# Performance work log

Measured on AMD Instinct MI355X. Metric: run time of the kernel, lower is better.

Reference implementation:

```python
import jax, jax.numpy as jnp
import numpy as np

D_MODEL = 768
D_STATE = 16
D_CONV = 4
EXPAND = 2
INNER = EXPAND * D_MODEL  # 1536
BATCH = 2
SEQLEN = 2048


def setup_inputs() -> dict:
    key = jax.random.key(0)
    ks = jax.random.split(key, 8)
    s = 0.02
    return {
        "hidden_states": jax.random.normal(ks[0], (BATCH, SEQLEN, D_MODEL), jnp.float32),
        "in_proj_w": jax.random.normal(ks[1], (2 * INNER, D_MODEL), jnp.float32) * (D_MODEL ** -0.5),
        "out_proj_w": jax.random.normal(ks[2], (D_MODEL, INNER), jnp.float32) * (INNER ** -0.5),
        "dt_proj_w": jax.random.normal(ks[3], (INNER, INNER), jnp.float32) * (INNER ** -0.5),
        "dt_proj_b": jnp.zeros((INNER,), jnp.float32),
        "conv_w": jax.random.normal(ks[4], (INNER, D_CONV), jnp.float32) * s,
        "conv_b": jnp.zeros((INNER,), jnp.float32),
        "A_log": jnp.zeros((INNER, D_STATE), jnp.float32),
        "B_param": jax.random.normal(ks[5], (INNER, D_STATE), jnp.float32) * s,
        "C_param": jax.random.normal(ks[6], (INNER, D_STATE), jnp.float32) * s,
        "D_param": jnp.ones((INNER,), jnp.float32),
        "dt_bias": jnp.zeros((INNER,), jnp.float32),
    }


def reference(hidden_states, in_proj_w, out_proj_w, dt_proj_w, dt_proj_b,
              conv_w, conv_b, A_log, B_param, C_param, D_param, dt_bias):
    # in_proj: (B, L, d_model) -> (B, L, 2*inner); split into projected / gate
    xz = jnp.einsum('bld,od->blo', hidden_states, in_proj_w)
    proj, gate = jnp.split(xz, 2, axis=-1)
    x = jnp.transpose(proj, (0, 2, 1))  # (B, inner, L) channel-first

    # depthwise causal conv (left-pad d_conv-1) + bias + SiLU
    conv = jax.lax.conv_general_dilated(
        x, conv_w[:, None, :], window_strides=(1,),
        padding=[(D_CONV - 1, 0)], feature_group_count=INNER,
        dimension_numbers=('NCH', 'OIH', 'NCH'))
    u = jax.nn.silu(conv + conv_b[None, :, None])  # (B, inner, L)

    # dt projection (1x1 linear on channel-first) + softplus(dt + dt_bias)
    delta = jnp.einsum('oc,bcl->bol', dt_proj_w, u) + dt_proj_b[None, :, None]
    dt = jax.nn.softplus(delta + dt_bias[None, :, None])  # (B, inner, L)

    A = -jnp.exp(A_log)  # (inner, d_state)
    # discretize: dA = exp(dt * A), dBu = dt * u * B   -> (B, inner, L, N)
    dA = jnp.exp(dt[..., None] * A[None, :, None, :])
    dBu = (dt * u)[..., None] * B_param[None, :, None, :]

    dA_t = jnp.moveaxis(dA, 2, 0)    # (L, B, inner, N)
    dBu_t = jnp.moveaxis(dBu, 2, 0)  # (L, B, inner, N)

    def step(h, inp):
        a_t, b_t = inp
        h = a_t * h + b_t                      # (B, inner, N)
        y = jnp.einsum('bdn,dn->bd', h, C_param)
        return h, y

    h0 = jnp.zeros(dA_t.shape[1:], dA.dtype)
    _, ys = jax.lax.scan(step, h0, (dA_t, dBu_t))  # ys: (L, B, inner)
    y = jnp.transpose(ys, (1, 2, 0))               # (B, inner, L)

    z = jnp.transpose(gate, (0, 2, 1))             # (B, inner, L)
    y = (y + D_param[None, :, None] * u) * jax.nn.silu(z)

    # out_proj: (B, inner, L) -> (B, L, d_model)
    return jnp.einsum('bdl,od->blo', y, out_proj_w)
```

## Files before the change

kernel.cpp:

```cpp
#include <hip/hip_runtime.h>
#include <cstdint>
#include <cstddef>

#define D_MODEL 768
#define D_STATE 16
#define D_CONV  4
#define INNER   1536
#define BATCH   2
#define SEQLEN  2048
#define M_TOK   (BATCH * SEQLEN)
#define NCH     (BATCH * INNER)
#define NCHUNK  128
#define CL      (SEQLEN / NCHUNK)

typedef unsigned short u16;
typedef __attribute__((ext_vector_type(4))) unsigned short us4;
typedef __attribute__((ext_vector_type(8))) short bf8;
typedef __attribute__((ext_vector_type(4))) float f32x4;
typedef __attribute__((ext_vector_type(4))) int i32x4;

#define INV254 (1.f / 254.f)

__device__ __forceinline__ u16 f2bf(float f) {
    uint32_t x = __float_as_uint(f);
    return (u16)((x + 0x7fffu + ((x >> 16) & 1u)) >> 16);
}
__device__ __forceinline__ float bf2f(u16 h) {
    return __uint_as_float(((uint32_t)h) << 16);
}
__device__ __forceinline__ int pk8(float a, float b, float c, float d) {
    return ((int)a & 0xff) | (((int)b & 0xff) << 8) |
           (((int)c & 0xff) << 16) | (((int)d & 0xff) << 24);
}

__global__ __launch_bounds__(256) void prep_all(
    const float* __restrict__ hs, int8_t* __restrict__ hs1, int8_t* __restrict__ hs0, float* __restrict__ sc_hs,
    const float* __restrict__ iw, int8_t* __restrict__ iw1, int8_t* __restrict__ iw0, float* __restrict__ sc_iw,
    const float* __restrict__ dw, int8_t* __restrict__ dw1, int8_t* __restrict__ dw0, float* __restrict__ sc_dw,
    const float* __restrict__ ow, u16* __restrict__ owh, u16* __restrict__ owl)
{
    const int blk = blockIdx.x;
    const int tid = threadIdx.x;

    if (blk >= M_TOK + 2 * INNER + INNER) {
        const int j = (blk - (M_TOK + 3 * INNER)) * 256 + tid;
        const int n4 = D_MODEL * INNER / 4;
        if (j >= n4) return;
        const float4 v = ((const float4*)ow)[j];
        us4 h, l;
        h.x = f2bf(v.x); l.x = f2bf(v.x - bf2f(h.x));
        h.y = f2bf(v.y); l.y = f2bf(v.y - bf2f(h.y));
        h.z = f2bf(v.z); l.z = f2bf(v.z - bf2f(h.z));
        h.w = f2bf(v.w); l.w = f2bf(v.w - bf2f(h.w));
        ((us4*)owh)[j] = h;
        ((us4*)owl)[j] = l;
        return;
    }

    const float* src; int8_t* q1; int8_t* q0; float* sc; int K; int row;
    if (blk < M_TOK) {
        src = hs; q1 = hs1; q0 = hs0; sc = sc_hs; K = D_MODEL; row = blk;
    } else if (blk < M_TOK + 2 * INNER) {
        src = iw; q1 = iw1; q0 = iw0; sc = sc_iw; K = D_MODEL; row = blk - M_TOK;
    } else {
        src = dw; q1 = dw1; q0 = dw0; sc = sc_dw; K = INNER; row = blk - M_TOK - 2 * INNER;
    }

    const float* r = src + (size_t)row * K;
    float mx = 0.f;
    for (int i = tid * 4; i < K; i += 1024) {
        const float4 v = *(const float4*)(r + i);
        mx = fmaxf(mx, fmaxf(fmaxf(fabsf(v.x), fabsf(v.y)),
                             fmaxf(fabsf(v.z), fabsf(v.w))));
    }
#pragma unroll
    for (int off = 1; off < 64; off <<= 1)
        mx = fmaxf(mx, __shfl_xor(mx, off, 64));
    __shared__ float red[4];
    if ((tid & 63) == 0) red[tid >> 6] = mx;
    __syncthreads();
    const float rm = fmaxf(fmaxf(red[0], red[1]), fmaxf(red[2], red[3]));
    const float q = rm > 0.f ? 127.f / rm : 0.f;

    for (int i = tid * 4; i < K; i += 1024) {
        const float4 v = *(const float4*)(r + i);
        float s1[4], s0[4];
        const float xv[4] = {v.x, v.y, v.z, v.w};
#pragma unroll
        for (int e = 0; e < 4; ++e) {
            const float t = xv[e] * q;
            s1[e] = rintf(t);
            s0[e] = rintf((t - s1[e]) * 254.f);
        }
        const size_t o = ((size_t)row * K + i) >> 2;
        ((int*)q1)[o] = pk8(s1[0], s1[1], s1[2], s1[3]);
        ((int*)q0)[o] = pk8(s0[0], s0[1], s0[2], s0[3]);
    }
    if (tid == 0) sc[row] = rm * (1.f / 127.f);
}

template <int MODE, int FRM, int FRN>
__global__ __launch_bounds__(256) void gemm_i8(
    const int8_t* __restrict__ A1g, const int8_t* __restrict__ A0g,
    const int8_t* __restrict__ B1g, const int8_t* __restrict__ B0g,
    const float* __restrict__ scA, const float* __restrict__ scB,
    void* __restrict__ Cv, const float* __restrict__ bias1,
    const float* __restrict__ bias2, int M, int N, int K)
{
    constexpr int BM = FRM * 32;
    constexpr int BN = FRN * 32;
    constexpr int SBUF = (BM + BN) * 128;
    __shared__ __align__(16) char smem[2 * SBUF];

    const int tid = threadIdx.x;
    const int w = tid >> 6;
    const int lane = tid & 63;

    const int gx = gridDim.x;
    const int nwg = gx * gridDim.y;
    int f = blockIdx.y * gx + blockIdx.x;
    f = (f & 7) * (nwg >> 3) + (f >> 3);
    const int bm = (f / gx) * BM;
    const int bn = (f % gx) * BN;

    const int wm = (w >> 1) * (FRM * 16);
    const int wn = (w & 1) * (FRN * 16);

    const int g8 = lane & 7;
    const int r8 = lane >> 3;
    const int srcg = g8 ^ r8;
    const int sbyte = (srcg & 3) * 16;
    const bool use_lo = (srcg & 4) != 0;

    const int8_t* pA[FRM];
    const int8_t* pB[FRN];
#pragma unroll
    for (int c = 0; c < FRM; ++c) {
        const int row = w * (FRM * 8) + c * 8 + r8;
        pA[c] = (use_lo ? A0g : A1g) + (size_t)(bm + row) * K + sbyte;
    }
#pragma unroll
    for (int c = 0; c < FRN; ++c) {
        const int row = w * (FRN * 8) + c * 8 + r8;
        pB[c] = (use_lo ? B0g : B1g) + (size_t)(bn + row) * K + sbyte;
    }

    i32x4 acc1[FRM][FRN] = {};
    i32x4 acc2[FRM][FRN] = {};
    const int fr = lane & 15;
    const int gk = lane >> 4;
    const int ghi = gk ^ (fr & 7);

    const int aoff1 = (wm + fr) * 128 + ghi * 16;
    const int aoff0 = (wm + fr) * 128 + (ghi ^ 4) * 16;
    const int boff1 = BM * 128 + (wn + fr) * 128 + ghi * 16;
    const int boff0 = BM * 128 + (wn + fr) * 128 + (ghi ^ 4) * 16;
    const char* const S0 = smem;
    const char* const S1 = smem + SBUF;

    const int nt = K >> 6;

#define STAGE_ALL(sb, kt)                                                           \
    {                                                                               \
        _Pragma("unroll")                                                           \
        for (int c = 0; c < FRM; ++c)                                               \
            __builtin_amdgcn_global_load_lds(                                       \
                (const __attribute__((address_space(1))) void*)(pA[c] + (kt)),      \
                (__attribute__((address_space(3))) void*)((char*)(sb) + (w * FRM + c) * 1024), \
                16, 0, 0);                                                          \
        _Pragma("unroll")                                                           \
        for (int c = 0; c < FRN; ++c)                                               \
            __builtin_amdgcn_global_load_lds(                                       \
                (const __attribute__((address_space(1))) void*)(pB[c] + (kt)),      \
                (__attribute__((address_space(3))) void*)((char*)(sb) + BM * 128 + (w * FRN + c) * 1024), \
                16, 0, 0);                                                          \
    }

#define WAIT_COUNTED()                                                              \
    if constexpr (FRM + FRN == 8) { asm volatile("s_waitcnt vmcnt(8)" ::: "memory"); } \
    else if constexpr (FRM + FRN == 6) { asm volatile("s_waitcnt vmcnt(6)" ::: "memory"); } \
    else { asm volatile("s_waitcnt vmcnt(4)" ::: "memory"); }

#define COMPUTE(S)                                                                  \
    {                                                                               \
        i32x4 a1[FRM], a0[FRM], b1[FRN], b0[FRN];                                   \
        _Pragma("unroll")                                                           \
        for (int i = 0; i < FRM; ++i) {                                             \
            a1[i] = *(const i32x4*)((S) + aoff1 + i * 2048);                        \
            a0[i] = *(const i32x4*)((S) + aoff0 + i * 2048);                        \
        }                                                                           \
        _Pragma("unroll")                                                           \
        for (int j = 0; j < FRN; ++j) {                                             \
            b1[j] = *(const i32x4*)((S) + boff1 + j * 2048);                        \
            b0[j] = *(const i32x4*)((S) + boff0 + j * 2048);                        \
        }                                                                           \
        _Pragma("unroll")                                                           \
        for (int i = 0; i < FRM; ++i)                                               \
            _Pragma("unroll")                                                       \
            for (int j = 0; j < FRN; ++j) {                                         \
                acc1[i][j] = __builtin_amdgcn_mfma_i32_16x16x64_i8(a1[i], b1[j], acc1[i][j], 0, 0, 0); \
                acc2[i][j] = __builtin_amdgcn_mfma_i32_16x16x64_i8(a1[i], b0[j], acc2[i][j], 0, 0, 0); \
                acc2[i][j] = __builtin_amdgcn_mfma_i32_16x16x64_i8(a0[i], b1[j], acc2[i][j], 0, 0, 0); \
            }                                                                       \
    }

    STAGE_ALL(S0, 0)

    for (int t = 0; t < nt; t += 2) {
        STAGE_ALL(S1, (t + 1) * 64)
        WAIT_COUNTED()
        __builtin_amdgcn_s_barrier();
        __builtin_amdgcn_sched_barrier(0);
        __builtin_amdgcn_s_setprio(1);
        COMPUTE(S0)
        __builtin_amdgcn_s_setprio(0);
        __builtin_amdgcn_sched_barrier(0);
        __builtin_amdgcn_s_barrier();

        const int k2 = (t + 2 < nt) ? (t + 2) * 64 : (nt - 1) * 64;
        STAGE_ALL(S0, k2)
        WAIT_COUNTED()
        __builtin_amdgcn_s_barrier();
        __builtin_amdgcn_sched_barrier(0);
        __builtin_amdgcn_s_setprio(1);
        COMPUTE(S1)
        __builtin_amdgcn_s_setprio(0);
        __builtin_amdgcn_sched_barrier(0);
        __builtin_amdgcn_s_barrier();
    }
#undef STAGE_ALL
#undef WAIT_COUNTED
#undef COMPUTE

    const int r0 = (lane >> 4) * 4;
#pragma unroll
    for (int i = 0; i < FRM; ++i) {
        const int row0 = bm + wm + i * 16 + r0;
        float sA[4];
#pragma unroll
        for (int r = 0; r < 4; ++r) sA[r] = scA[row0 + r];
#pragma unroll
        for (int j = 0; j < FRN; ++j) {
            const int col = bn + wn + j * 16 + fr;
            const float sB = scB[col];
            float add = 0.f;
            if constexpr (MODE == 1) add = bias1[col] + bias2[col];
#pragma unroll
            for (int r = 0; r < 4; ++r) {
                float v = ((float)acc1[i][j][r] +
                           (float)acc2[i][j][r] * INV254) * (sA[r] * sB);
                if constexpr (MODE == 1) {
                    const float xx = v + add;
                    v = (xx > 20.f) ? xx : log1pf(expf(xx));
                    ((u16*)Cv)[(size_t)(row0 + r) * N + col] = f2bf(v);
                } else {
                    ((float*)Cv)[(size_t)(row0 + r) * N + col] = v;
                }
            }
        }
    }
}

template <int MODE, int FRM, int FRN>
__global__ __launch_bounds__(256) void gemm_mfma(
    const u16* __restrict__ Ah_g, const u16* __restrict__ Al_g,
    const u16* __restrict__ Bh_g, const u16* __restrict__ Bl_g,
    float* __restrict__ C, const float* __restrict__ bias1,
    const float* __restrict__ bias2, int M, int N, int K)
{
    constexpr int BM = FRM * 32;
    constexpr int BN = FRN * 32;
    constexpr int SBUF = (BM + BN) * 128;
    __shared__ __align__(16) char smem[2 * SBUF];

    const int tid = threadIdx.x;
    const int w = tid >> 6;
    const int lane = tid & 63;

    const int gx = gridDim.x;
    const int nwg = gx * gridDim.y;
    int f = blockIdx.y * gx + blockIdx.x;
    f = (f & 7) * (nwg >> 3) + (f >> 3);
    const int bm = (f / gx) * BM;
    const int bn = (f % gx) * BN;

    const int wm = (w >> 1) * (FRM * 16);
    const int wn = (w & 1) * (FRN * 16);

    const int g8 = lane & 7;
    const int r8 = lane >> 3;
    const int srcg = g8 ^ r8;
    const int scol = (srcg & 3) * 8;
    const bool use_lo = (srcg & 4) != 0;

    const u16* pA[FRM];
    const u16* pB[FRN];
#pragma unroll
    for (int c = 0; c < FRM; ++c) {
        const int row = w * (FRM * 8) + c * 8 + r8;
        pA[c] = (use_lo ? Al_g : Ah_g) + (size_t)(bm + row) * K + scol;
    }
#pragma unroll
    for (int c = 0; c < FRN; ++c) {
        const int row = w * (FRN * 8) + c * 8 + r8;
        pB[c] = (use_lo ? Bl_g : Bh_g) + (size_t)(bn + row) * K + scol;
    }

    f32x4 acc[FRM][FRN] = {};
    const int fr = lane & 15;
    const int gk = lane >> 4;
    const int ghi = gk ^ (fr & 7);

    const int aoff_h = (wm + fr) * 128 + ghi * 16;
    const int aoff_l = (wm + fr) * 128 + (ghi ^ 4) * 16;
    const int boff_h = BM * 128 + (wn + fr) * 128 + ghi * 16;
    const int boff_l = BM * 128 + (wn + fr) * 128 + (ghi ^ 4) * 16;
    const char* const S0 = smem;
    const char* const S1 = smem + SBUF;

    const int nt = K >> 5;

#define STAGE_ALL(sb, kt)                                                           \
    {                                                                               \
        _Pragma("unroll")                                                           \
        for (int c = 0; c < FRM; ++c)                                               \
            __builtin_amdgcn_global_load_lds(                                       \
                (const __attribute__((address_space(1))) void*)(pA[c] + (kt)),      \
                (__attribute__((address_space(3))) void*)((char*)(sb) + (w * FRM + c) * 1024), \
                16, 0, 0);                                                          \
        _Pragma("unroll")                                                           \
        for (int c = 0; c < FRN; ++c)                                               \
            __builtin_amdgcn_global_load_lds(                                       \
                (const __attribute__((address_space(1))) void*)(pB[c] + (kt)),      \
                (__attribute__((address_space(3))) void*)((char*)(sb) + BM * 128 + (w * FRN + c) * 1024), \
                16, 0, 0);                                                          \
    }

#define WAIT_COUNTED()                                                              \
    if constexpr (FRM + FRN == 8) { asm volatile("s_waitcnt vmcnt(8)" ::: "memory"); } \
    else if constexpr (FRM + FRN == 6) { asm volatile("s_waitcnt vmcnt(6)" ::: "memory"); } \
    else { asm volatile("s_waitcnt vmcnt(4)" ::: "memory"); }

#define COMPUTE(S)                                                                  \
    {                                                                               \
        bf8 ah[FRM], al[FRM], bh[FRN], bl[FRN];                                     \
        _Pragma("unroll")                                                           \
        for (int i = 0; i < FRM; ++i) {                                             \
            ah[i] = *(const bf8*)((S) + aoff_h + i * 2048);                         \
            al[i] = *(const bf8*)((S) + aoff_l + i * 2048);                         \
        }                                                                           \
        _Pragma("unroll")                                                           \
        for (int j = 0; j < FRN; ++j) {                                             \
            bh[j] = *(const bf8*)((S) + boff_h + j * 2048);                         \
            bl[j] = *(const bf8*)((S) + boff_l + j * 2048);                         \
        }                                                                           \
        _Pragma("unroll")                                                           \
        for (int i = 0; i < FRM; ++i)                                               \
            _Pragma("unroll")                                                       \
            for (int j = 0; j < FRN; ++j) {                                         \
                acc[i][j] = __builtin_amdgcn_mfma_f32_16x16x32_bf16(ah[i], bh[j], acc[i][j], 0, 0, 0); \
                acc[i][j] = __builtin_amdgcn_mfma_f32_16x16x32_bf16(ah[i], bl[j], acc[i][j], 0, 0, 0); \
                acc[i][j] = __builtin_amdgcn_mfma_f32_16x16x32_bf16(al[i], bh[j], acc[i][j], 0, 0, 0); \
            }                                                                       \
    }

    STAGE_ALL(S0, 0)

    for (int t = 0; t < nt; t += 2) {
        STAGE_ALL(S1, (t + 1) * 32)
        WAIT_COUNTED()
        __builtin_amdgcn_s_barrier();
        __builtin_amdgcn_sched_barrier(0);
        __builtin_amdgcn_s_setprio(1);
        COMPUTE(S0)
        __builtin_amdgcn_s_setprio(0);
        __builtin_amdgcn_sched_barrier(0);
        __builtin_amdgcn_s_barrier();

        const int k2 = (t + 2 < nt) ? (t + 2) * 32 : (nt - 1) * 32;
        STAGE_ALL(S0, k2)
        WAIT_COUNTED()
        __builtin_amdgcn_s_barrier();
        __builtin_amdgcn_sched_barrier(0);
        __builtin_amdgcn_s_setprio(1);
        COMPUTE(S1)
        __builtin_amdgcn_s_setprio(0);
        __builtin_amdgcn_sched_barrier(0);
        __builtin_amdgcn_s_barrier();
    }
#undef STAGE_ALL
#undef WAIT_COUNTED
#undef COMPUTE

    const int r0 = (lane >> 4) * 4;
#pragma unroll
    for (int i = 0; i < FRM; ++i) {
        const int row0 = bm + wm + i * 16 + r0;
#pragma unroll
        for (int j = 0; j < FRN; ++j) {
            const int col = bn + wn + j * 16 + fr;
            float add = 0.f;
            if constexpr (MODE == 1) add = bias1[col] + bias2[col];
#pragma unroll
            for (int r = 0; r < 4; ++r) {
                float v = acc[i][j][r];
                if constexpr (MODE == 1) {
                    const float xx = v + add;
                    v = (xx > 20.f) ? xx : log1pf(expf(xx));
                }
                C[(size_t)(row0 + r) * N + col] = v;
            }
        }
    }
}

__global__ __launch_bounds__(384) void conv_silu_quant(
    const float* __restrict__ xz, const float* __restrict__ cw,
    const float* __restrict__ cb, int8_t* __restrict__ u1,
    int8_t* __restrict__ u0, float* __restrict__ su)
{
    const int m = blockIdx.x;
    const int tid = threadIdx.x;
    const int c4 = tid * 4;
    const int b = m >> 11;
    const int l = m & (SEQLEN - 1);

    float wt[4][4];
#pragma unroll
    for (int i = 0; i < 4; ++i) {
        const float4 wv = *(const float4*)&cw[(c4 + i) * 4];
        wt[i][0] = wv.x; wt[i][1] = wv.y; wt[i][2] = wv.z; wt[i][3] = wv.w;
    }
    const float4 bias = *(const float4*)&cb[c4];
    float a[4] = {bias.x, bias.y, bias.z, bias.w};

#pragma unroll
    for (int j = 0; j < 4; ++j) {
        const int ll = l - 3 + j;
        if (ll >= 0) {
            const float4 x = *(const float4*)&xz[(size_t)(b * SEQLEN + ll) * (2 * INNER) + c4];
            a[0] = fmaf(x.x, wt[0][j], a[0]);
            a[1] = fmaf(x.y, wt[1][j], a[1]);
            a[2] = fmaf(x.z, wt[2][j], a[2]);
            a[3] = fmaf(x.w, wt[3][j], a[3]);
        }
    }
    float o[4];
#pragma unroll
    for (int i = 0; i < 4; ++i) o[i] = a[i] / (1.f + __expf(-a[i]));

    float mx = fmaxf(fmaxf(fabsf(o[0]), fabsf(o[1])),
                     fmaxf(fabsf(o[2]), fabsf(o[3])));
#pragma unroll
    for (int off = 1; off < 64; off <<= 1)
        mx = fmaxf(mx, __shfl_xor(mx, off, 64));
    __shared__ float red[6];
    if ((tid & 63) == 0) red[tid >> 6] = mx;
    __syncthreads();
    float rm = red[0];
#pragma unroll
    for (int i = 1; i < 6; ++i) rm = fmaxf(rm, red[i]);
    const float q = rm > 0.f ? 127.f / rm : 0.f;

    float s1[4], s0[4];
#pragma unroll
    for (int e = 0; e < 4; ++e) {
        const float t = o[e] * q;
        s1[e] = rintf(t);
        s0[e] = rintf((t - s1[e]) * 254.f);
    }
    const size_t vi = ((size_t)m * INNER + c4) >> 2;
    ((int*)u1)[vi] = pk8(s1[0], s1[1], s1[2], s1[3]);
    ((int*)u0)[vi] = pk8(s0[0], s0[1], s0[2], s0[3]);
    if (tid == 0) su[m] = rm * (1.f / 127.f);
}

__global__ __launch_bounds__(256) void scan_pass1(
    const u16* __restrict__ dtb, const int8_t* __restrict__ u1,
    const int8_t* __restrict__ u0, const float* __restrict__ su,
    const float* __restrict__ A_log, const float* __restrict__ Bp,
    float* __restrict__ hend, float* __restrict__ Sdt)
{
    const int ch = blockIdx.x * 256 + threadIdx.x;
    const int c = blockIdx.y;
    const int b = (ch >= INNER) ? 1 : 0;
    const int d = ch - b * INNER;

    float A2[D_STATE], Bn[D_STATE];
#pragma unroll
    for (int n = 0; n < D_STATE; n += 4) {
        const float4 av = *(const float4*)&A_log[d * D_STATE + n];
        const float4 bv = *(const float4*)&Bp[d * D_STATE + n];
        A2[n+0] = -expf(av.x) * 1.44269504f; Bn[n+0] = bv.x;
        A2[n+1] = -expf(av.y) * 1.44269504f; Bn[n+1] = bv.y;
        A2[n+2] = -expf(av.z) * 1.44269504f; Bn[n+2] = bv.z;
        A2[n+3] = -expf(av.w) * 1.44269504f; Bn[n+3] = bv.w;
    }

    const size_t base = (size_t)(b * SEQLEN + c * CL) * INNER + d;
    const u16* dtp = dtb + base;
    const int8_t* u1p = u1 + base;
    const int8_t* u0p = u0 + base;
    const float* sup = su + (b * SEQLEN + c * CL);

    float h[D_STATE] = {};
    float S = 0.f;

    float dtv = bf2f(dtp[0]);
    float uv = fmaf((float)u0p[0], INV254, (float)u1p[0]) * sup[0];

    for (int l = 0; l < CL; ++l) {
        float dtn = 0.f, un = 0.f;
        if (l + 1 < CL) {
            dtn = bf2f(dtp[(size_t)(l + 1) * INNER]);
            un = fmaf((float)u0p[(size_t)(l + 1) * INNER], INV254,
                      (float)u1p[(size_t)(l + 1) * INNER]) * sup[l + 1];
        }
        const float dtu = dtv * uv;
        S += dtv;
#pragma unroll
        for (int n = 0; n < D_STATE; ++n) {
            const float dA = exp2f(dtv * A2[n]);
            h[n] = fmaf(dA, h[n], dtu * Bn[n]);
        }
        dtv = dtn; uv = un;
    }

#pragma unroll
    for (int n = 0; n < D_STATE; ++n)
        hend[((size_t)c * D_STATE + n) * NCH + ch] = h[n];
    Sdt[(size_t)c * NCH + ch] = S;
}

__global__ __launch_bounds__(256) void scan_combine(
    const float* __restrict__ hend, const float* __restrict__ Sdt,
    const float* __restrict__ A_log, float* __restrict__ h0all)
{
    const int idx = blockIdx.x * 256 + threadIdx.x;
    const int n = idx / NCH;
    const int ch = idx - n * NCH;
    const int b = (ch >= INNER) ? 1 : 0;
    const int d = ch - b * INNER;
    const float A2 = -expf(A_log[d * D_STATE + n]) * 1.44269504f;

    float h0 = 0.f;
    for (int c = 0; c < NCHUNK; ++c) {
        const size_t o = ((size_t)c * D_STATE + n) * NCH + ch;
        h0all[o] = h0;
        const float P = exp2f(A2 * Sdt[(size_t)c * NCH + ch]);
        h0 = fmaf(P, h0, hend[o]);
    }
}

__global__ __launch_bounds__(256) void scan_pass2(
    const u16* __restrict__ dtb, const int8_t* __restrict__ u1,
    const int8_t* __restrict__ u0, const float* __restrict__ su,
    const float* __restrict__ xz, const float* __restrict__ A_log,
    const float* __restrict__ Bp, const float* __restrict__ Cp,
    const float* __restrict__ Dp, const float* __restrict__ h0all,
    u16* __restrict__ ygh, u16* __restrict__ ygl)
{
    const int ch = blockIdx.x * 256 + threadIdx.x;
    const int c = blockIdx.y;
    const int b = (ch >= INNER) ? 1 : 0;
    const int d = ch - b * INNER;

    float A2[D_STATE], Bn[D_STATE], Cn[D_STATE];
#pragma unroll
    for (int n = 0; n < D_STATE; n += 4) {
        const float4 av = *(const float4*)&A_log[d * D_STATE + n];
        const float4 bv = *(const float4*)&Bp[d * D_STATE + n];
        const float4 cv = *(const float4*)&Cp[d * D_STATE + n];
        A2[n+0] = -expf(av.x) * 1.44269504f; Bn[n+0] = bv.x; Cn[n+0] = cv.x;
        A2[n+1] = -expf(av.y) * 1.44269504f; Bn[n+1] = bv.y; Cn[n+1] = cv.y;
        A2[n+2] = -expf(av.z) * 1.44269504f; Bn[n+2] = bv.z; Cn[n+2] = cv.z;
        A2[n+3] = -expf(av.w) * 1.44269504f; Bn[n+3] = bv.w; Cn[n+3] = cv.w;
    }
    const float Dd = Dp[d];

    float h[D_STATE];
#pragma unroll
    for (int n = 0; n < D_STATE; ++n)
        h[n] = h0all[((size_t)c * D_STATE + n) * NCH + ch];

    const size_t base = (size_t)(b * SEQLEN + c * CL) * INNER + d;
    const u16* dtp = dtb + base;
    const int8_t* u1p = u1 + base;
    const int8_t* u0p = u0 + base;
    const float* sup = su + (b * SEQLEN + c * CL);
    const float* zp = xz + (size_t)(b * SEQLEN + c * CL) * (2 * INNER) + INNER + d;
    u16* yhp = ygh + base;
    u16* ylp = ygl + base;

    float dtv = bf2f(dtp[0]);
    float uv = fmaf((float)u0p[0], INV254, (float)u1p[0]) * sup[0];
    float zv = zp[0];

    for (int l = 0; l < CL; ++l) {
        float dtn = 0.f, un = 0.f, zn = 0.f;
        if (l + 1 < CL) {
            dtn = bf2f(dtp[(size_t)(l + 1) * INNER]);
            un = fmaf((float)u0p[(size_t)(l + 1) * INNER], INV254,
                      (float)u1p[(size_t)(l + 1) * INNER]) * sup[l + 1];
            zn = zp[(size_t)(l + 1) * (2 * INNER)];
        }
        const float dtu = dtv * uv;
        float y = 0.f;
#pragma unroll
        for (int n = 0; n < D_STATE; ++n) {
            const float dA = exp2f(dtv * A2[n]);
            h[n] = fmaf(dA, h[n], dtu * Bn[n]);
            y = fmaf(h[n], Cn[n], y);
        }
        const float sig = 1.f / (1.f + __expf(-zv));
        const float val = (y + Dd * uv) * (zv * sig);
        const u16 hv = f2bf(val);
        yhp[(size_t)l * INNER] = hv;
        ylp[(size_t)l * INNER] = f2bf(val - bf2f(hv));
        dtv = dtn; uv = un; zv = zn;
    }
}

extern "C" void kernel_launch(void* const* d_in, const int* in_sizes, int n_in,
                              void* d_out, int out_size, void* d_ws, size_t ws_size,
                              hipStream_t stream)
{
    const float* hs      = (const float*)d_in[0];
    const float* in_w    = (const float*)d_in[1];
    const float* out_w   = (const float*)d_in[2];
    const float* dt_w    = (const float*)d_in[3];
    const float* dt_b    = (const float*)d_in[4];
    const float* conv_w  = (const float*)d_in[5];
    const float* conv_b  = (const float*)d_in[6];
    const float* A_log   = (const float*)d_in[7];
    const float* Bp      = (const float*)d_in[8];
    const float* Cp      = (const float*)d_in[9];
    const float* Dp      = (const float*)d_in[10];
    const float* dt_bias = (const float*)d_in[11];
    float* out = (float*)d_out;

    float* xz    = (float*)d_ws;
    float* hend  = xz + (size_t)M_TOK * 2 * INNER;
    float* Sdt   = hend + (size_t)NCHUNK * D_STATE * NCH;
    float* h0all = Sdt + (size_t)NCHUNK * NCH;
    float* su_u  = h0all + (size_t)NCHUNK * D_STATE * NCH;
    float* sc_hs = su_u + M_TOK;
    float* sc_iw = sc_hs + M_TOK;
    float* sc_dw = sc_iw + 2 * INNER;
    u16* dtb = (u16*)(sc_dw + INNER);
    u16* ygh = dtb + (size_t)M_TOK * INNER;
    u16* ygl = ygh + (size_t)M_TOK * INNER;
    u16* owh = ygl + (size_t)M_TOK * INNER;
    u16* owl = owh + (size_t)D_MODEL * INNER;
    int8_t* hs1 = (int8_t*)(owl + (size_t)D_MODEL * INNER);
    int8_t* hs0 = hs1 + (size_t)M_TOK * D_MODEL;
    int8_t* iw1 = hs0 + (size_t)M_TOK * D_MODEL;
    int8_t* iw0 = iw1 + (size_t)2 * INNER * D_MODEL;
    int8_t* dw1 = iw0 + (size_t)2 * INNER * D_MODEL;
    int8_t* dw0 = dw1 + (size_t)INNER * INNER;
    int8_t* u1  = dw0 + (size_t)INNER * INNER;
    int8_t* u0  = u1 + (size_t)M_TOK * INNER;

    const dim3 blk(256);

    {
        const int nq = M_TOK + 2 * INNER + INNER;
        const int nc = (D_MODEL * INNER / 4 + 255) / 256;
        prep_all<<<dim3(nq + nc), blk, 0, stream>>>(
            hs, hs1, hs0, sc_hs, in_w, iw1, iw0, sc_iw,
            dt_w, dw1, dw0, sc_dw, out_w, owh, owl);
    }

    gemm_i8<0, 4, 4><<<dim3(2 * INNER / 128, M_TOK / 128), blk, 0, stream>>>(
        hs1, hs0, iw1, iw0, sc_hs, sc_iw, xz, nullptr, nullptr,
        M_TOK, 2 * INNER, D_MODEL);

    conv_silu_quant<<<dim3(M_TOK), dim3(384), 0, stream>>>(
        xz, conv_w, conv_b, u1, u0, su_u);

    gemm_i8<1, 4, 2><<<dim3(INNER / 64, M_TOK / 128), blk, 0, stream>>>(
        u1, u0, dw1, dw0, su_u, sc_dw, dtb, dt_b, dt_bias,
        M_TOK, INNER, INNER);

    scan_pass1<<<dim3(NCH / 256, NCHUNK), blk, 0, stream>>>(
        dtb, u1, u0, su_u, A_log, Bp, hend, Sdt);
    scan_combine<<<dim3((D_STATE * NCH) / 256), blk, 0, stream>>>(
        hend, Sdt, A_log, h0all);
    scan_pass2<<<dim3(NCH / 256, NCHUNK), blk, 0, stream>>>(
        dtb, u1, u0, su_u, xz, A_log, Bp, Cp, Dp, h0all, ygh, ygl);

    gemm_mfma<0, 2, 2><<<dim3(D_MODEL / 64, M_TOK / 64), blk, 0, stream>>>(
        ygh, ygl, owh, owl, out, nullptr, nullptr, M_TOK, D_MODEL, INNER);
}
```

Before: 306.0 us.

## Switch out_proj GEMM from split-bf16 MFMA to two-level int8 GEMM

```diff
diff --git a/kernel.cpp b/kernel.cpp
--- a/kernel.cpp
+++ b/kernel.cpp
@@ -15,7 +15,6 @@
 
 typedef unsigned short u16;
 typedef __attribute__((ext_vector_type(4))) unsigned short us4;
-typedef __attribute__((ext_vector_type(8))) short bf8;
 typedef __attribute__((ext_vector_type(4))) float f32x4;
 typedef __attribute__((ext_vector_type(4))) int i32x4;
 
@@ -33,40 +32,11 @@
            (((int)c & 0xff) << 16) | (((int)d & 0xff) << 24);
 }
 
-__global__ __launch_bounds__(256) void prep_all(
-    const float* __restrict__ hs, int8_t* __restrict__ hs1, int8_t* __restrict__ hs0, float* __restrict__ sc_hs,
-    const float* __restrict__ iw, int8_t* __restrict__ iw1, int8_t* __restrict__ iw0, float* __restrict__ sc_iw,
-    const float* __restrict__ dw, int8_t* __restrict__ dw1, int8_t* __restrict__ dw0, float* __restrict__ sc_dw,
-    const float* __restrict__ ow, u16* __restrict__ owh, u16* __restrict__ owl)
-{
-    const int blk = blockIdx.x;
-    const int tid = threadIdx.x;
-
-    if (blk >= M_TOK + 2 * INNER + INNER) {
-        const int j = (blk - (M_TOK + 3 * INNER)) * 256 + tid;
-        const int n4 = D_MODEL * INNER / 4;
-        if (j >= n4) return;
-        const float4 v = ((const float4*)ow)[j];
-        us4 h, l;
-        h.x = f2bf(v.x); l.x = f2bf(v.x - bf2f(h.x));
-        h.y = f2bf(v.y); l.y = f2bf(v.y - bf2f(h.y));
-        h.z = f2bf(v.z); l.z = f2bf(v.z - bf2f(h.z));
-        h.w = f2bf(v.w); l.w = f2bf(v.w - bf2f(h.w));
-        ((us4*)owh)[j] = h;
-        ((us4*)owl)[j] = l;
-        return;
-    }
-
-    const float* src; int8_t* q1; int8_t* q0; float* sc; int K; int row;
-    if (blk < M_TOK) {
-        src = hs; q1 = hs1; q0 = hs0; sc = sc_hs; K = D_MODEL; row = blk;
-    } else if (blk < M_TOK + 2 * INNER) {
-        src = iw; q1 = iw1; q0 = iw0; sc = sc_iw; K = D_MODEL; row = blk - M_TOK;
-    } else {
-        src = dw; q1 = dw1; q0 = dw0; sc = sc_dw; K = INNER; row = blk - M_TOK - 2 * INNER;
-    }
-
-    const float* r = src + (size_t)row * K;
+__device__ __forceinline__ void rowquant_body(
+    const float* __restrict__ r, int8_t* __restrict__ q1,
+    int8_t* __restrict__ q0, float* __restrict__ sc,
+    int K, size_t rowbase, int tid)
+{
     float mx = 0.f;
     for (int i = tid * 4; i < K; i += 1024) {
         const float4 v = *(const float4*)(r + i);
@@ -92,11 +62,42 @@
             s1[e] = rintf(t);
             s0[e] = rintf((t - s1[e]) * 254.f);
         }
-        const size_t o = ((size_t)row * K + i) >> 2;
+        const size_t o = (rowbase + i) >> 2;
         ((int*)q1)[o] = pk8(s1[0], s1[1], s1[2], s1[3]);
         ((int*)q0)[o] = pk8(s0[0], s0[1], s0[2], s0[3]);
     }
-    if (tid == 0) sc[row] = rm * (1.f / 127.f);
+    if (tid == 0) *sc = rm * (1.f / 127.f);
+}
+
+__global__ __launch_bounds__(256) void prep_all(
+    const float* __restrict__ hs, int8_t* __restrict__ hs1, int8_t* __restrict__ hs0, float* __restrict__ sc_hs,
+    const float* __restrict__ iw, int8_t* __restrict__ iw1, int8_t* __restrict__ iw0, float* __restrict__ sc_iw,
+    const float* __restrict__ dw, int8_t* __restrict__ dw1, int8_t* __restrict__ dw0, float* __restrict__ sc_dw,
+    const float* __restrict__ ow, int8_t* __restrict__ ow1, int8_t* __restrict__ ow0, float* __restrict__ sc_ow)
+{
+    const int blk = blockIdx.x;
+    const int tid = threadIdx.x;
+    const float* src; int8_t* q1; int8_t* q0; float* sc; int K; int row;
+    if (blk < M_TOK) {
+        src = hs; q1 = hs1; q0 = hs0; sc = sc_hs; K = D_MODEL; row = blk;
+    } else if (blk < M_TOK + 2 * INNER) {
+        src = iw; q1 = iw1; q0 = iw0; sc = sc_iw; K = D_MODEL; row = blk - M_TOK;
+    } else if (blk < M_TOK + 3 * INNER) {
+        src = dw; q1 = dw1; q0 = dw0; sc = sc_dw; K = INNER; row = blk - M_TOK - 2 * INNER;
+    } else {
+        src = ow; q1 = ow1; q0 = ow0; sc = sc_ow; K = INNER; row = blk - M_TOK - 3 * INNER;
+    }
+    rowquant_body(src + (size_t)row * K, q1, q0, sc + row, K,
+                  (size_t)row * K, tid);
+}
+
+__global__ __launch_bounds__(256) void rowquant_yg(
+    const float* __restrict__ src, int8_t* __restrict__ q1,
+    int8_t* __restrict__ q0, float* __restrict__ sc)
+{
+    const int row = blockIdx.x;
+    rowquant_body(src + (size_t)row * INNER, q1, q0, sc + row, INNER,
+                  (size_t)row * INNER, threadIdx.x);
 }
 
 template <int MODE, int FRM, int FRN>
@@ -261,159 +262,6 @@
     }
 }
 
-template <int MODE, int FRM, int FRN>
-__global__ __launch_bounds__(256) void gemm_mfma(
-    const u16* __restrict__ Ah_g, const u16* __restrict__ Al_g,
-    const u16* __restrict__ Bh_g, const u16* __restrict__ Bl_g,
-    float* __restrict__ C, const float* __restrict__ bias1,
-    const float* __restrict__ bias2, int M, int N, int K)
-{
-    constexpr int BM = FRM * 32;
-    constexpr int BN = FRN * 32;
-    constexpr int SBUF = (BM + BN) * 128;
-    __shared__ __align__(16) char smem[2 * SBUF];
-
-    const int tid = threadIdx.x;
-    const int w = tid >> 6;
-    const int lane = tid & 63;
-
-    const int gx = gridDim.x;
-    const int nwg = gx * gridDim.y;
-    int f = blockIdx.y * gx + blockIdx.x;
-    f = (f & 7) * (nwg >> 3) + (f >> 3);
-    const int bm = (f / gx) * BM;
-    const int bn = (f % gx) * BN;
-
-    const int wm = (w >> 1) * (FRM * 16);
-    const int wn = (w & 1) * (FRN * 16);
-
-    const int g8 = lane & 7;
-    const int r8 = lane >> 3;
-    const int srcg = g8 ^ r8;
-    const int scol = (srcg & 3) * 8;
-    const bool use_lo = (srcg & 4) != 0;
-
-    const u16* pA[FRM];
-    const u16* pB[FRN];
-#pragma unroll
-    for (int c = 0; c < FRM; ++c) {
-        const int row = w * (FRM * 8) + c * 8 + r8;
-        pA[c] = (use_lo ? Al_g : Ah_g) + (size_t)(bm + row) * K + scol;
-    }
-#pragma unroll
-    for (int c = 0; c < FRN; ++c) {
-        const int row = w * (FRN * 8) + c * 8 + r8;
-        pB[c] = (use_lo ? Bl_g : Bh_g) + (size_t)(bn + row) * K + scol;
-    }
-
-    f32x4 acc[FRM][FRN] = {};
-    const int fr = lane & 15;
-    const int gk = lane >> 4;
-    const int ghi = gk ^ (fr & 7);
-
-    const int aoff_h = (wm + fr) * 128 + ghi * 16;
-    const int aoff_l = (wm + fr) * 128 + (ghi ^ 4) * 16;
-    const int boff_h = BM * 128 + (wn + fr) * 128 + ghi * 16;
-    const int boff_l = BM * 128 + (wn + fr) * 128 + (ghi ^ 4) * 16;
-    const char* const S0 = smem;
-    const char* const S1 = smem + SBUF;
-
-    const int nt = K >> 5;
-
-#define STAGE_ALL(sb, kt)                                                           \
-    {                                                                               \
-        _Pragma("unroll")                                                           \
-        for (int c = 0; c < FRM; ++c)                                               \
-            __builtin_amdgcn_global_load_lds(                                       \
-                (const __attribute__((address_space(1))) void*)(pA[c] + (kt)),      \
-                (__attribute__((address_space(3))) void*)((char*)(sb) + (w * FRM + c) * 1024), \
-                16, 0, 0);                                                          \
-        _Pragma("unroll")                                                           \
-        for (int c = 0; c < FRN; ++c)                                               \
-            __builtin_amdgcn_global_load_lds(                                       \
-                (const __attribute__((address_space(1))) void*)(pB[c] + (kt)),      \
-                (__attribute__((address_space(3))) void*)((char*)(sb) + BM * 128 + (w * FRN + c) * 1024), \
-                16, 0, 0);                                                          \
-    }
-
-#define WAIT_COUNTED()                                                              \
-    if constexpr (FRM + FRN == 8) { asm volatile("s_waitcnt vmcnt(8)" ::: "memory"); } \
-    else if constexpr (FRM + FRN == 6) { asm volatile("s_waitcnt vmcnt(6)" ::: "memory"); } \
-    else { asm volatile("s_waitcnt vmcnt(4)" ::: "memory"); }
-
-#define COMPUTE(S)                                                                  \
-    {                                                                               \
-        bf8 ah[FRM], al[FRM], bh[FRN], bl[FRN];                                     \
-        _Pragma("unroll")                                                           \
-        for (int i = 0; i < FRM; ++i) {                                             \
-            ah[i] = *(const bf8*)((S) + aoff_h + i * 2048);                         \
-            al[i] = *(const bf8*)((S) + aoff_l + i * 2048);                         \
-        }                                                                           \
-        _Pragma("unroll")                                                           \
-        for (int j = 0; j < FRN; ++j) {                                             \
-            bh[j] = *(const bf8*)((S) + boff_h + j * 2048);                         \
-            bl[j] = *(const bf8*)((S) + boff_l + j * 2048);                         \
-        }                                                                           \
-        _Pragma("unroll")                                                           \
-        for (int i = 0; i < FRM; ++i)                                               \
-            _Pragma("unroll")                                                       \
-            for (int j = 0; j < FRN; ++j) {                                         \
-                acc[i][j] = __builtin_amdgcn_mfma_f32_16x16x32_bf16(ah[i], bh[j], acc[i][j], 0, 0, 0); \
-                acc[i][j] = __builtin_amdgcn_mfma_f32_16x16x32_bf16(ah[i], bl[j], acc[i][j], 0, 0, 0); \
-                acc[i][j] = __builtin_amdgcn_mfma_f32_16x16x32_bf16(al[i], bh[j], acc[i][j], 0, 0, 0); \
-            }                                                                       \
-    }
-
-    STAGE_ALL(S0, 0)
-
-    for (int t = 0; t < nt; t += 2) {
-        STAGE_ALL(S1, (t + 1) * 32)
-        WAIT_COUNTED()
-        __builtin_amdgcn_s_barrier();
-        __builtin_amdgcn_sched_barrier(0);
-        __builtin_amdgcn_s_setprio(1);
-        COMPUTE(S0)
-        __builtin_amdgcn_s_setprio(0);
-        __builtin_amdgcn_sched_barrier(0);
-        __builtin_amdgcn_s_barrier();
-
-        const int k2 = (t + 2 < nt) ? (t + 2) * 32 : (nt - 1) * 32;
-        STAGE_ALL(S0, k2)
-        WAIT_COUNTED()
-        __builtin_amdgcn_s_barrier();
-        __builtin_amdgcn_sched_barrier(0);
-        __builtin_amdgcn_s_setprio(1);
-        COMPUTE(S1)
-        __builtin_amdgcn_s_setprio(0);
-        __builtin_amdgcn_sched_barrier(0);
-        __builtin_amdgcn_s_barrier();
-    }
-#undef STAGE_ALL
-#undef WAIT_COUNTED
-#undef COMPUTE
-
-    const int r0 = (lane >> 4) * 4;
-#pragma unroll
-    for (int i = 0; i < FRM; ++i) {
-        const int row0 = bm + wm + i * 16 + r0;
-#pragma unroll
-        for (int j = 0; j < FRN; ++j) {
-            const int col = bn + wn + j * 16 + fr;
-            float add = 0.f;
-            if constexpr (MODE == 1) add = bias1[col] + bias2[col];
-#pragma unroll
-            for (int r = 0; r < 4; ++r) {
-                float v = acc[i][j][r];
-                if constexpr (MODE == 1) {
-                    const float xx = v + add;
-                    v = (xx > 20.f) ? xx : log1pf(expf(xx));
-                }
-                C[(size_t)(row0 + r) * N + col] = v;
-            }
-        }
-    }
-}
-
 __global__ __launch_bounds__(384) void conv_silu_quant(
     const float* __restrict__ xz, const float* __restrict__ cw,
     const float* __restrict__ cb, int8_t* __restrict__ u1,
@@ -558,7 +406,7 @@
     const float* __restrict__ xz, const float* __restrict__ A_log,
     const float* __restrict__ Bp, const float* __restrict__ Cp,
     const float* __restrict__ Dp, const float* __restrict__ h0all,
-    u16* __restrict__ ygh, u16* __restrict__ ygl)
+    float* __restrict__ yg)
 {
     const int ch = blockIdx.x * 256 + threadIdx.x;
     const int c = blockIdx.y;
@@ -589,8 +437,7 @@
     const int8_t* u0p = u0 + base;
     const float* sup = su + (b * SEQLEN + c * CL);
     const float* zp = xz + (size_t)(b * SEQLEN + c * CL) * (2 * INNER) + INNER + d;
-    u16* yhp = ygh + base;
-    u16* ylp = ygl + base;
+    float* ygp = yg + base;
 
     float dtv = bf2f(dtp[0]);
     float uv = fmaf((float)u0p[0], INV254, (float)u1p[0]) * sup[0];
@@ -613,10 +460,7 @@
             y = fmaf(h[n], Cn[n], y);
         }
         const float sig = 1.f / (1.f + __expf(-zv));
-        const float val = (y + Dd * uv) * (zv * sig);
-        const u16 hv = f2bf(val);
-        yhp[(size_t)l * INNER] = hv;
-        ylp[(size_t)l * INNER] = f2bf(val - bf2f(hv));
+        ygp[(size_t)l * INNER] = (y + Dd * uv) * (zv * sig);
         dtv = dtn; uv = un; zv = zn;
     }
 }
@@ -643,35 +487,34 @@
     float* hend  = xz + (size_t)M_TOK * 2 * INNER;
     float* Sdt   = hend + (size_t)NCHUNK * D_STATE * NCH;
     float* h0all = Sdt + (size_t)NCHUNK * NCH;
-    float* su_u  = h0all + (size_t)NCHUNK * D_STATE * NCH;
+    float* yg    = h0all + (size_t)NCHUNK * D_STATE * NCH;
+    float* su_u  = yg + (size_t)M_TOK * INNER;
     float* sc_hs = su_u + M_TOK;
     float* sc_iw = sc_hs + M_TOK;
     float* sc_dw = sc_iw + 2 * INNER;
-    u16* dtb = (u16*)(sc_dw + INNER);
-    u16* ygh = dtb + (size_t)M_TOK * INNER;
-    u16* ygl = ygh + (size_t)M_TOK * INNER;
-    u16* owh = ygl + (size_t)M_TOK * INNER;
-    u16* owl = owh + (size_t)D_MODEL * INNER;
-    int8_t* hs1 = (int8_t*)(owl + (size_t)D_MODEL * INNER);
+    float* sc_ow = sc_dw + INNER;
+    float* sc_yg = sc_ow + D_MODEL;
+    u16* dtb = (u16*)(sc_yg + M_TOK);
+    int8_t* hs1 = (int8_t*)(dtb + (size_t)M_TOK * INNER);
     int8_t* hs0 = hs1 + (size_t)M_TOK * D_MODEL;
     int8_t* iw1 = hs0 + (size_t)M_TOK * D_MODEL;
     int8_t* iw0 = iw1 + (size_t)2 * INNER * D_MODEL;
     int8_t* dw1 = iw0 + (size_t)2 * INNER * D_MODEL;
     int8_t* dw0 = dw1 + (size_t)INNER * INNER;
-    int8_t* u1  = dw0 + (size_t)INNER * INNER;
+    int8_t* ow1 = dw0 + (size_t)INNER * INNER;
+    int8_t* ow0 = ow1 + (size_t)D_MODEL * INNER;
+    int8_t* u1  = ow0 + (size_t)D_MODEL * INNER;
     int8_t* u0  = u1 + (size_t)M_TOK * INNER;
+    int8_t* yg1 = u0 + (size_t)M_TOK * INNER;
+    int8_t* yg0 = yg1 + (size_t)M_TOK * INNER;
 
     const dim3 blk(256);
 
-    {
-        const int nq = M_TOK + 2 * INNER + INNER;
-        const int nc = (D_MODEL * INNER / 4 + 255) / 256;
-        prep_all<<<dim3(nq + nc), blk, 0, stream>>>(
-            hs, hs1, hs0, sc_hs, in_w, iw1, iw0, sc_iw,
-            dt_w, dw1, dw0, sc_dw, out_w, owh, owl);
-    }
-
-    gemm_i8<0, 4, 4><<<dim3(2 * INNER / 128, M_TOK / 128), blk, 0, stream>>>(
+    prep_all<<<dim3(M_TOK + 3 * INNER + D_MODEL), blk, 0, stream>>>(
+        hs, hs1, hs0, sc_hs, in_w, iw1, iw0, sc_iw,
+        dt_w, dw1, dw0, sc_dw, out_w, ow1, ow0, sc_ow);
+
+    gemm_i8<0, 4, 2><<<dim3(2 * INNER / 64, M_TOK / 128), blk, 0, stream>>>(
         hs1, hs0, iw1, iw0, sc_hs, sc_iw, xz, nullptr, nullptr,
         M_TOK, 2 * INNER, D_MODEL);
 
@@ -687,8 +530,11 @@
     scan_combine<<<dim3((D_STATE * NCH) / 256), blk, 0, stream>>>(
         hend, Sdt, A_log, h0all);
     scan_pass2<<<dim3(NCH / 256, NCHUNK), blk, 0, stream>>>(
-        dtb, u1, u0, su_u, xz, A_log, Bp, Cp, Dp, h0all, ygh, ygl);
-
-    gemm_mfma<0, 2, 2><<<dim3(D_MODEL / 64, M_TOK / 64), blk, 0, stream>>>(
-        ygh, ygl, owh, owl, out, nullptr, nullptr, M_TOK, D_MODEL, INNER);
-}
+        dtb, u1, u0, su_u, xz, A_log, Bp, Cp, Dp, h0all, yg);
+
+    rowquant_yg<<<dim3(M_TOK), blk, 0, stream>>>(yg, yg1, yg0, sc_yg);
+
+    gemm_i8<0, 2, 2><<<dim3(D_MODEL / 64, M_TOK / 64), blk, 0, stream>>>(
+        yg1, yg0, ow1, ow0, sc_yg, sc_ow, out, nullptr, nullptr,
+        M_TOK, D_MODEL, INNER);
+}
```

Measured after the change: 285.0 us. 6.9% less time.
